# Performance work log

Hardware: AMD Instinct MI355X
Metric: run time of the kernel (lower is better)

## Reference

```python
import jax, jax.numpy as jnp
import numpy as np

B_SI = 4.1491   # neutron scattering length Si (fm)
B_O = 5.803     # neutron scattering length O (fm)
CUTOFF = 3.5    # tetrahedral neighbour cutoff (A)
BIG = 1e6       # masked-distance sentinel (finite to keep grads NaN-free)


def setup_inputs() -> dict:
    key = jax.random.key(0)
    k1, k2 = jax.random.split(key)
    N, L = 4096, 40.0
    positions = jax.random.uniform(k1, (N, 3), dtype=jnp.float32) * L
    cell = (L * jnp.eye(3)).astype(jnp.float32)
    r_bins = (0.05 + 0.05 * jnp.arange(200, dtype=jnp.float32))      # 0.05..10.0 A
    q_bins = jnp.linspace(0.5, 25.0, 500, dtype=jnp.float32)          # A^-1
    species = jax.random.randint(k2, (N,), 0, 3, dtype=jnp.int32)     # 0=Si, 1/2=O
    return {"positions": positions, "cell": cell, "r_bins": r_bins,
            "q_bins": q_bins, "species": species}


def _pair_geometry(positions, cell):
    # Minimum-image displacements under a general periodic cell.
    disp = positions[:, None, :] - positions[None, :, :]        # [N,N,3]
    frac = disp @ jnp.linalg.inv(cell)
    frac = frac - jnp.round(frac)
    disp = frac @ cell
    d2 = jnp.sum(disp * disp, axis=-1)                           # [N,N]
    self_mask = jnp.eye(positions.shape[0], dtype=bool)
    dist = jnp.sqrt(jnp.where(self_mask, 1.0, d2))               # safe sqrt on diag
    return disp, dist, self_mask


def reference(positions, cell, r_bins, q_bins, species):
    N = positions.shape[0]
    nbins = r_bins.shape[0]
    dtype = positions.dtype

    disp, dist, self_mask = _pair_geometry(positions, cell)

    # --- neutron-weighted G(r): differentiable linear (cloud-in-cell) binning ---
    b = jnp.where(species == 0, B_SI, B_O).astype(dtype)         # per-atom scattering length
    w = (b[:, None] * b[None, :]) / (jnp.mean(b) ** 2)           # Faber-Ziman pair weights
    r0, dr = r_bins[0], r_bins[1] - r_bins[0]
    x = (dist - r0) / dr
    i0 = jnp.floor(x).astype(jnp.int32)
    f = x - i0.astype(dtype)
    valid = (~self_mask) & (i0 >= 0) & (i0 < nbins - 1)
    w0 = jnp.where(valid, w * (1.0 - f), 0.0).ravel()
    w1 = jnp.where(valid, w * f, 0.0).ravel()
    i0f = jnp.clip(i0, 0, nbins - 1).ravel()
    hist = (jnp.zeros(nbins, dtype)
            .at[i0f].add(w0)
            .at[jnp.clip(i0f + 1, 0, nbins - 1)].add(w1))
    V = jnp.abs(jnp.linalg.det(cell))
    rho = N / V
    shell = 4.0 * jnp.pi * r_bins ** 2 * dr                       # ideal-gas shell volume
    G_r = hist / (N * rho * shell)                                # [nbins]

    # --- total correlation function T(r) = 4 pi rho r G(r) ---
    T_r = 4.0 * jnp.pi * rho * r_bins * G_r

    # --- structure factor S(Q) = 1 + 4 pi rho int r^2 (G(r)-1) sinc(Qr) dr ---
    qr = q_bins[:, None] * r_bins[None, :]                        # [nQ, nr]
    integrand = (r_bins ** 2) * (G_r - 1.0)
    S_Q = 1.0 + 4.0 * jnp.pi * rho * dr * jnp.sum(
        integrand[None, :] * jnp.sinc(qr / jnp.pi), axis=1)

    # --- tetrahedral order parameter q_tet over Si centres with O neighbours ---
    central = species == 0
    nbr_ok = (species != 0)[None, :] & (~self_mask)
    nd = jnp.where(nbr_ok, dist, BIG)
    negd, idx = jax.lax.top_k(-nd, 4)                             # 4 nearest O per atom
    d4 = -negd                                                    # [N,4]
    u = jnp.take_along_axis(disp, idx[:, :, None], axis=1) / d4[:, :, None]  # unit vecs
    cosang = jnp.einsum('nkd,nld->nkl', u, u)                     # [N,4,4]
    pair_mask = jnp.triu(jnp.ones((4, 4), bool), 1)               # 6 angle pairs
    q_i = 1.0 - (3.0 / 8.0) * jnp.sum(((cosang + 1.0 / 3.0) ** 2) * pair_mask, axis=(1, 2))
    vf = (central & (d4[:, 3] < CUTOFF)).astype(dtype)            # needs 4 nbrs in cutoff
    q_tet = jnp.sum(q_i * vf) / jnp.maximum(jnp.sum(vf), 1.0)

    return G_r, T_r, S_Q, q_tet
```

## Files before the change

### kernel.cpp

```cpp
#include <hip/hip_runtime.h>
#include <climits>
#include <math.h>


#define B_SI_F 4.1491f
#define B_O_F  5.803f
#define CUTOFF_F 3.5f
#define CUT_SLACK 3.5005f
#define NCOPIES 16
#define CAP 32

#define WS_HIST 16
#define WS_CNT  4096

__device__ __forceinline__ bool dless(float da, int ia, float db, int ib) {
    return (da < db) || (da == db && ia < ib);
}

struct CellK {
    float ci0, ci1, ci2, ci3, ci4, ci5, ci6, ci7, ci8;
    float c0, c1, c2, c3, c4, c5, c6, c7, c8;
};

__device__ __forceinline__ CellK make_cell(const float* __restrict__ cellm,
                                           bool& diag) {
    CellK K;
    K.c0 = cellm[0]; K.c1 = cellm[1]; K.c2 = cellm[2];
    K.c3 = cellm[3]; K.c4 = cellm[4]; K.c5 = cellm[5];
    K.c6 = cellm[6]; K.c7 = cellm[7]; K.c8 = cellm[8];
    double m0 = K.c0, m1 = K.c1, m2 = K.c2;
    double m3 = K.c3, m4 = K.c4, m5 = K.c5;
    double m6 = K.c6, m7 = K.c7, m8 = K.c8;
    double det = m0*(m4*m8 - m5*m7) - m1*(m3*m8 - m5*m6) + m2*(m3*m7 - m4*m6);
    double rd = 1.0 / det;
    K.ci0 = (float)( (m4*m8 - m5*m7) * rd);
    K.ci1 = (float)(-(m1*m8 - m2*m7) * rd);
    K.ci2 = (float)( (m1*m5 - m2*m4) * rd);
    K.ci3 = (float)(-(m3*m8 - m5*m6) * rd);
    K.ci4 = (float)( (m0*m8 - m2*m6) * rd);
    K.ci5 = (float)(-(m0*m5 - m2*m3) * rd);
    K.ci6 = (float)( (m3*m7 - m4*m6) * rd);
    K.ci7 = (float)(-(m0*m7 - m1*m6) * rd);
    K.ci8 = (float)( (m0*m4 - m1*m3) * rd);
    diag = (K.c1 == 0.0f) && (K.c2 == 0.0f) && (K.c3 == 0.0f) &&
           (K.c5 == 0.0f) && (K.c6 == 0.0f) && (K.c7 == 0.0f);
    return K;
}

template<bool DIAG>
__device__ __forceinline__ void min_image(const CellK& K,
                                          float dx, float dy, float dz,
                                          float& ex, float& ey, float& ez) {
    if (DIAG) {
        float t0 = dx * K.ci0, t1 = dy * K.ci4, t2 = dz * K.ci8;
        t0 -= rintf(t0);  t1 -= rintf(t1);  t2 -= rintf(t2);
        ex = t0 * K.c0;  ey = t1 * K.c4;  ez = t2 * K.c8;
    } else {
        float f0 = dx*K.ci0 + dy*K.ci3 + dz*K.ci6;
        float f1 = dx*K.ci1 + dy*K.ci4 + dz*K.ci7;
        float f2 = dx*K.ci2 + dy*K.ci5 + dz*K.ci8;
        f0 -= rintf(f0);  f1 -= rintf(f1);  f2 -= rintf(f2);
        ex = f0*K.c0 + f1*K.c3 + f2*K.c6;
        ey = f0*K.c1 + f1*K.c4 + f2*K.c7;
        ez = f0*K.c2 + f1*K.c5 + f2*K.c8;
    }
}

template<bool DIAG>
__device__ __forceinline__ void hist_sweep(const CellK& K,
                                           const float4* __restrict__ sj,
                                           int lbase, int jb0,
                                           float xi, float yi, float zi, float wi,
                                           float rb0, float inv_dr, int nbins_m1,
                                           float* shist,
                                           bool iSi, bool iO, bool offdiag, int iidx,
                                           float* __restrict__ cnt,
                                           int* __restrict__ cand) {
    #pragma unroll 4
    for (int l = 0; l < 32; ++l) {
        const float4 pj = sj[lbase + l];
        float ex, ey, ez;
        min_image<DIAG>(K, xi - pj.x, yi - pj.y, zi - pj.z, ex, ey, ez);
        float dist = __builtin_amdgcn_sqrtf(fmaf(ex, ex, fmaf(ey, ey, ez * ez)));
        float x  = (dist - rb0) * inv_dr;
        float fl = floorf(x);
        int   i0 = (int)fl;
        if (i0 >= 0 && i0 < nbins_m1) {
            float w = wi * pj.w;
            float f = x - fl;
            atomicAdd(&shist[i0],     w * (1.0f - f));
            atomicAdd(&shist[i0 + 1], w * f);
        }
        if (dist < CUT_SLACK) {
            const int jg = jb0 + lbase + l;
            if (iSi && pj.w == B_O_F) {
                float old = atomicAdd(&cnt[iidx], 1.0f);
                int slot = (int)rintf(old);
                if (slot < CAP) cand[iidx * CAP + slot] = jg;
            }
            if (offdiag && iO && pj.w == B_SI_F) {
                float old = atomicAdd(&cnt[jg], 1.0f);
                int slot = (int)rintf(old);
                if (slot < CAP) cand[jg * CAP + slot] = iidx;
            }
        }
    }
}

__global__ __launch_bounds__(256) void k_main(const float* __restrict__ cellm,
                                              const float* __restrict__ pos,
                                              const int* __restrict__ species,
                                              const float* __restrict__ rbins,
                                              float* __restrict__ ws,
                                              int N, int nbins, int T) {
    const int tid = threadIdx.x;
    const int bid = blockIdx.x;

    bool diag;
    const CellK K = make_cell(cellm, diag);

    __shared__ float shist[256];
    __shared__ float sjf[64 * 4];
    shist[tid] = 0.0f;

    const int jhalf = bid & 1;
    int rem = bid >> 1;
    int ti = 0;
    while (rem >= T - ti) { rem -= T - ti; ti++; }
    const int tj = ti + rem;
    const int jb0 = tj * 128 + jhalf * 64;

    if (tid < 192) {
        int g = 3 * jb0 + tid;
        float v = (g < 3 * N) ? pos[g] : 0.0f;
        sjf[(tid / 3) * 4 + (tid % 3)] = v;
    } else {
        int a = tid - 192;
        int ja = jb0 + a;
        float b = (ja < N) ? ((species[ja] == 0) ? B_SI_F : B_O_F) : 0.0f;
        sjf[a * 4 + 3] = b;
    }

    const float rb0     = rbins[0];
    const float inv_dr  = 1.0f / (rbins[1] - rbins[0]);
    const int   nbins_m1 = nbins - 1;

    const int il  = tid & 127;
    const int sub = tid >> 7;
    const int i   = ti * 128 + il;
    const int ig  = min(i, N - 1);
    const float xi = pos[3*ig], yi = pos[3*ig+1], zi = pos[3*ig+2];
    const int   spi = species[ig];
    const float b_i = (spi == 0) ? B_SI_F : B_O_F;
    const float wmul = (ti == tj) ? 1.0f : 2.0f;
    const float wi = (i < N) ? b_i * wmul : 0.0f;
    const bool iSi = (i < N) && (spi == 0);
    const bool iO  = (i < N) && (spi != 0);
    const bool offdiag = (ti != tj);

    float* cnt  = ws + WS_CNT;
    int*   cand = (int*)(ws + WS_CNT + 3 * (size_t)N);

    __syncthreads();

    const float4* sj = (const float4*)sjf;
    if (diag) hist_sweep<true >(K, sj, sub * 32, jb0, xi, yi, zi, wi, rb0, inv_dr, nbins_m1, shist, iSi, iO, offdiag, i, cnt, cand);
    else      hist_sweep<false>(K, sj, sub * 32, jb0, xi, yi, zi, wi, rb0, inv_dr, nbins_m1, shist, iSi, iO, offdiag, i, cnt, cand);

    __syncthreads();

    float* gh = ws + WS_HIST + (size_t)(bid % NCOPIES) * nbins;
    for (int t = tid; t < nbins; t += 256) {
        float h = shist[t];
        if (h != 0.0f) atomicAdd(&gh[t], h);
    }
}

template<bool DIAG>
__device__ __forceinline__ void top4_sweep_s(const CellK& K,
                                             const float* __restrict__ pos,
                                             const int* __restrict__ species,
                                             int N, int lane, int self,
                                             float xi, float yi, float zi,
                                             float& e0, float& e1, float& e2, float& e3,
                                             int& j0, int& j1, int& j2, int& j3) {
    for (int k = lane; k < N; k += 64) {
        int   sp = species[k];
        float px = pos[3*k], py = pos[3*k+1], pz = pos[3*k+2];
        float ex, ey, ez;
        min_image<DIAG>(K, xi - px, yi - py, zi - pz, ex, ey, ez);
        float d2 = fmaf(ex, ex, fmaf(ey, ey, ez * ez));
        float c  = (sp != 0 && k != self) ? d2 : 1e30f;
        int   jc = k;
        if (dless(c, jc, e3, j3)) {
            bool lt2 = dless(c, jc, e2, j2);
            bool lt1 = dless(c, jc, e1, j1);
            bool lt0 = dless(c, jc, e0, j0);
            e3 = lt2 ? e2 : c;               j3 = lt2 ? j2 : jc;
            e2 = lt2 ? (lt1 ? e1 : c) : e2;  j2 = lt2 ? (lt1 ? j1 : jc) : j2;
            e1 = lt1 ? (lt0 ? e0 : c) : e1;  j1 = lt1 ? (lt0 ? j0 : jc) : j1;
            e0 = lt0 ? c : e0;               j0 = lt0 ? jc : j0;
        }
    }
}

__global__ __launch_bounds__(256) void k_tet(const float* __restrict__ cellm,
                                             const float* __restrict__ pos,
                                             const int* __restrict__ species,
                                             float* __restrict__ ws, int N) {
    const int s = __builtin_amdgcn_readfirstlane(blockIdx.x * 4 + (threadIdx.x >> 6));
    if (s >= N) return;
    const int lane = threadIdx.x & 63;

    float* cnt = ws + WS_CNT;
    float* qv  = ws + WS_CNT + N;
    const int* cand = (const int*)(ws + WS_CNT + 3 * (size_t)N);

    if (species[s] != 0) {
        if (lane == 0) { qv[2*s] = 0.0f; qv[2*s + 1] = 0.0f; }
        return;
    }

    bool diag;
    const CellK K = make_cell(cellm, diag);
    const float xi = pos[3*s], yi = pos[3*s+1], zi = pos[3*s+2];

    const int c = (int)rintf(cnt[s]);
    if (lane == 0) cnt[s] = 0.0f;

    float e0 = 1e30f, e1 = 1e30f, e2 = 1e30f, e3 = 1e30f;
    int   j0 = INT_MAX, j1 = INT_MAX, j2 = INT_MAX, j3 = INT_MAX;

    if (c <= CAP) {
        if (lane < c) {
            int j = cand[s * CAP + lane];
            float ex, ey, ez;
            if (diag) min_image<true >(K, xi - pos[3*j], yi - pos[3*j+1], zi - pos[3*j+2], ex, ey, ez);
            else      min_image<false>(K, xi - pos[3*j], yi - pos[3*j+1], zi - pos[3*j+2], ex, ey, ez);
            e0 = fmaf(ex, ex, fmaf(ey, ey, ez * ez));
            j0 = j;
        }
    } else {
        if (diag) top4_sweep_s<true >(K, pos, species, N, lane, s, xi, yi, zi, e0, e1, e2, e3, j0, j1, j2, j3);
        else      top4_sweep_s<false>(K, pos, species, N, lane, s, xi, yi, zi, e0, e1, e2, e3, j0, j1, j2, j3);
    }

    float r0d, r1d, r2d, r3d;  int r0j, r1j, r2j, r3j;
    #define EXTRACT_MIN(RD, RJ)                                        \
    {                                                                  \
        float md = e0; int mj = j0;                                    \
        for (int off = 32; off > 0; off >>= 1) {                       \
            float od = __shfl_xor(md, off, 64);                        \
            int   oj = __shfl_xor(mj, off, 64);                        \
            bool keep = dless(md, mj, od, oj);                         \
            md = keep ? md : od;                                       \
            mj = keep ? mj : oj;                                       \
        }                                                              \
        RD = md; RJ = mj;                                              \
        bool pop = (j0 == mj);                                         \
        e0 = pop ? e1 : e0;  j0 = pop ? j1 : j0;                       \
        e1 = pop ? e2 : e1;  j1 = pop ? j2 : j1;                       \
        e2 = pop ? e3 : e2;  j2 = pop ? j3 : j2;                       \
        e3 = pop ? 1e30f : e3;  j3 = pop ? INT_MAX : j3;               \
    }
    EXTRACT_MIN(r0d, r0j)
    EXTRACT_MIN(r1d, r1j)
    EXTRACT_MIN(r2d, r2j)
    EXTRACT_MIN(r3d, r3j)
    #undef EXTRACT_MIN

    if (lane == 0) {
        float qiv = 0.0f, vf = 0.0f;
        if (r3j != INT_MAX) {
            float dd0 = sqrtf(r0d), dd1 = sqrtf(r1d), dd2 = sqrtf(r2d), dd3 = sqrtf(r3d);
            if (dd3 < CUTOFF_F) {
                float ux[4], uy[4], uz[4];
                float dd[4]  = {dd0, dd1, dd2, dd3};
                int   jj4[4] = {r0j, r1j, r2j, r3j};
                #pragma unroll
                for (int k = 0; k < 4; ++k) {
                    int jk = jj4[k];
                    float ex, ey, ez;
                    if (diag) min_image<true >(K, xi - pos[3*jk], yi - pos[3*jk+1], zi - pos[3*jk+2], ex, ey, ez);
                    else      min_image<false>(K, xi - pos[3*jk], yi - pos[3*jk+1], zi - pos[3*jk+2], ex, ey, ez);
                    ux[k] = ex / dd[k];
                    uy[k] = ey / dd[k];
                    uz[k] = ez / dd[k];
                }
                float s2 = 0.0f;
                #pragma unroll
                for (int k = 0; k < 4; ++k)
                    #pragma unroll
                    for (int l = k + 1; l < 4; ++l) {
                        float cs = ux[k]*ux[l] + uy[k]*uy[l] + uz[k]*uz[l];
                        float t  = cs + (1.0f / 3.0f);
                        s2 += t * t;
                    }
                qiv = 1.0f - 0.375f * s2;
                vf  = 1.0f;
            }
        }
        qv[2*s]     = qiv;
        qv[2*s + 1] = vf;
    }
}

__device__ __forceinline__ float fast_sinc(float x) {
    float rev = x * 0.15915494309189535f;
    rev -= rintf(rev);
    float sn = __builtin_amdgcn_sinf(rev);
    return sn * __builtin_amdgcn_rcpf(x);
}

__global__ __launch_bounds__(256) void k_finalize(const float* __restrict__ cellm,
                                                  const float* __restrict__ ws,
                                                  const float* __restrict__ rbins,
                                                  const float* __restrict__ qbins,
                                                  const int* __restrict__ species,
                                                  float* __restrict__ out,
                                                  int N, int nbins, int nq) {
    __shared__ float2 srw[256];
    __shared__ float rq[256], rv[256];
    __shared__ int   scnt[256];
    const int tid = threadIdx.x;

    double m0 = cellm[0], m1 = cellm[1], m2 = cellm[2];
    double m3 = cellm[3], m4 = cellm[4], m5 = cellm[5];
    double m6 = cellm[6], m7 = cellm[7], m8 = cellm[8];
    double det = m0*(m4*m8 - m5*m7) - m1*(m3*m8 - m5*m6) + m2*(m3*m7 - m4*m6);
    const float rho = (float)((double)N / fabs(det));

    {
        int c = 0;
        for (int k = tid; k < N; k += 256) c += (species[k] == 0) ? 1 : 0;
        scnt[tid] = c;
    }
    __syncthreads();
    for (int s = 128; s > 0; s >>= 1) {
        if (tid < s) scnt[tid] += scnt[tid + s];
        __syncthreads();
    }
    const int nSi = scnt[0];
    const float mean_b  = ((float)nSi * B_SI_F + (float)(N - nSi) * B_O_F) / (float)N;
    const float w_scale = 1.0f / (mean_b * mean_b);

    const float dr  = rbins[1] - rbins[0];
    const float FOURPI = 4.0f * 3.14159265358979323846f;

    for (int t = tid; t < nbins; t += blockDim.x) {
        float h = 0.0f;
        #pragma unroll
        for (int c = 0; c < NCOPIES; ++c) h += ws[WS_HIST + c * nbins + t];
        h *= w_scale;
        float r = rbins[t];
        float shell = FOURPI * r * r * dr;
        float g = h / ((float)N * rho * shell);
        srw[t] = make_float2(r, r * r * (g - 1.0f));
        if (blockIdx.x == 0) {
            out[t] = g;
            out[nbins + t] = FOURPI * rho * r * g;
        }
    }

    if (blockIdx.x == 0) {
        const float* qv = ws + WS_CNT + N;
        float sq = 0.0f, sv = 0.0f;
        for (int s = tid; s < N; s += 256) {
            sq += qv[2*s];
            sv += qv[2*s + 1];
        }
        rq[tid] = sq; rv[tid] = sv;
    }
    __syncthreads();
    if (blockIdx.x == 0) {
        for (int s = 128; s > 0; s >>= 1) {
            if (tid < s) { rq[tid] += rq[tid + s]; rv[tid] += rv[tid + s]; }
            __syncthreads();
        }
        if (tid == 0)
            out[2 * nbins + nq] = rq[0] / fmaxf(rv[0], 1.0f);
    }

    int q = blockIdx.x * blockDim.x + tid;
    if (q < nq) {
        float qq = qbins[q];
        float s0 = 0.0f, s1 = 0.0f, s2 = 0.0f, s3 = 0.0f;
        int t = 0;
        for (; t + 4 <= nbins; t += 4) {
            float2 a = srw[t], b = srw[t+1], c = srw[t+2], d = srw[t+3];
            s0 += a.y * fast_sinc(qq * a.x);
            s1 += b.y * fast_sinc(qq * b.x);
            s2 += c.y * fast_sinc(qq * c.x);
            s3 += d.y * fast_sinc(qq * d.x);
        }
        for (; t < nbins; ++t) {
            float2 a = srw[t];
            s0 += a.y * fast_sinc(qq * a.x);
        }
        float s = (s0 + s1) + (s2 + s3);
        out[2 * nbins + q] = 1.0f + FOURPI * rho * dr * s;
    }
}

extern "C" void kernel_launch(void* const* d_in, const int* in_sizes, int n_in,
                              void* d_out, int out_size, void* d_ws, size_t ws_size,
                              hipStream_t stream) {
    const float* pos     = (const float*)d_in[0];
    const float* cell    = (const float*)d_in[1];
    const float* rbins   = (const float*)d_in[2];
    const float* qbins   = (const float*)d_in[3];
    const int*   species = (const int*)d_in[4];
    float* out = (float*)d_out;
    float* ws  = (float*)d_ws;

    const int N     = in_sizes[4];
    const int nbins = in_sizes[2];
    const int nq    = in_sizes[3];

    const int T  = (N + 127) / 128;
    const int P2 = T * (T + 1);
    const int BT = (N + 3) / 4;
    const int QB = (nq + 255) / 256;

    k_main<<<P2, 256, 0, stream>>>(cell, pos, species, rbins, ws, N, nbins, T);
    k_tet<<<BT, 256, 0, stream>>>(cell, pos, species, ws, N);
    k_finalize<<<QB, 256, 0, stream>>>(cell, ws, rbins, qbins, species, out, N, nbins, nq);
}
```

Measured before the change: 96.84 us.

## Fuse tet kernel into finalize, precompute fractional coords, replicate shared histograms

The main pair kernel now handles a full 128x128 tile per block with half the blocks. It precomputes fractional coordinates for both atom sets so each pair needs only a subtract and rint. Shared-memory histogram atomics are spread across four replicas to reduce contention, and the neighbour cutoff test uses squared distance. The separate q_tet kernel is merged into the finalize launch as extra blocks that reduce through global atomics with a last-block counter, removing one launch and the per-atom q buffer. The extra workspace counters must reset correctly across calls, and the larger tiles mean fewer blocks to fill the device.

```diff
diff --git a/kernel.cpp b/kernel.cpp
--- a/kernel.cpp
+++ b/kernel.cpp
@@ -6,7 +6,7 @@
 #define B_SI_F 4.1491f
 #define B_O_F  5.803f
 #define CUTOFF_F 3.5f
-#define CUT_SLACK 3.5005f
+#define CS2 12.25350025f
 #define NCOPIES 16
 #define CAP 32
 
@@ -70,28 +70,38 @@
 __device__ __forceinline__ void hist_sweep(const CellK& K,
                                            const float4* __restrict__ sj,
                                            int lbase, int jb0,
-                                           float xi, float yi, float zi, float wi,
-                                           float rb0, float inv_dr, int nbins_m1,
-                                           float* shist,
+                                           float fi0, float fi1, float fi2,
+                                           float wi, float inv_dr, float nrb0,
+                                           int nbins_m1, float* shc,
                                            bool iSi, bool iO, bool offdiag, int iidx,
                                            float* __restrict__ cnt,
                                            int* __restrict__ cand) {
     #pragma unroll 4
-    for (int l = 0; l < 32; ++l) {
+    for (int l = 0; l < 64; ++l) {
         const float4 pj = sj[lbase + l];
+        float d0 = fi0 - pj.x;  d0 -= rintf(d0);
+        float d1 = fi1 - pj.y;  d1 -= rintf(d1);
+        float d2 = fi2 - pj.z;  d2 -= rintf(d2);
         float ex, ey, ez;
-        min_image<DIAG>(K, xi - pj.x, yi - pj.y, zi - pj.z, ex, ey, ez);
-        float dist = __builtin_amdgcn_sqrtf(fmaf(ex, ex, fmaf(ey, ey, ez * ez)));
-        float x  = (dist - rb0) * inv_dr;
+        if (DIAG) {
+            ex = d0 * K.c0;  ey = d1 * K.c4;  ez = d2 * K.c8;
+        } else {
+            ex = d0*K.c0 + d1*K.c3 + d2*K.c6;
+            ey = d0*K.c1 + d1*K.c4 + d2*K.c7;
+            ez = d0*K.c2 + d1*K.c5 + d2*K.c8;
+        }
+        float dsq  = fmaf(ex, ex, fmaf(ey, ey, ez * ez));
+        float dist = __builtin_amdgcn_sqrtf(dsq);
+        float x  = fmaf(dist, inv_dr, nrb0);
         float fl = floorf(x);
         int   i0 = (int)fl;
-        if (i0 >= 0 && i0 < nbins_m1) {
-            float w = wi * pj.w;
-            float f = x - fl;
-            atomicAdd(&shist[i0],     w * (1.0f - f));
-            atomicAdd(&shist[i0 + 1], w * f);
-        }
-        if (dist < CUT_SLACK) {
+        if ((unsigned)i0 < (unsigned)nbins_m1) {
+            float w  = wi * pj.w;
+            float wf = w * (x - fl);
+            atomicAdd(&shc[i0],     w - wf);
+            atomicAdd(&shc[i0 + 1], wf);
+        }
+        if (dsq < CS2) {
             const int jg = jb0 + lbase + l;
             if (iSi && pj.w == B_O_F) {
                 float old = atomicAdd(&cnt[iidx], 1.0f);
@@ -119,30 +129,40 @@
     bool diag;
     const CellK K = make_cell(cellm, diag);
 
-    __shared__ float shist[256];
-    __shared__ float sjf[64 * 4];
-    shist[tid] = 0.0f;
-
-    const int jhalf = bid & 1;
-    int rem = bid >> 1;
-    int ti = 0;
+    __shared__ float sh[4 * 257];
+    __shared__ float sjf[128 * 4];
+
+    for (int u = tid; u < 4 * 257; u += 256) sh[u] = 0.0f;
+
+    int rem = bid, ti = 0;
     while (rem >= T - ti) { rem -= T - ti; ti++; }
-    const int tj = ti + rem;
-    const int jb0 = tj * 128 + jhalf * 64;
-
-    if (tid < 192) {
-        int g = 3 * jb0 + tid;
-        float v = (g < 3 * N) ? pos[g] : 0.0f;
-        sjf[(tid / 3) * 4 + (tid % 3)] = v;
-    } else {
-        int a = tid - 192;
-        int ja = jb0 + a;
-        float b = (ja < N) ? ((species[ja] == 0) ? B_SI_F : B_O_F) : 0.0f;
-        sjf[a * 4 + 3] = b;
-    }
-
-    const float rb0     = rbins[0];
-    const float inv_dr  = 1.0f / (rbins[1] - rbins[0]);
+    const int tj  = ti + rem;
+    const int jb0 = tj * 128;
+
+    for (int u = tid; u < 384; u += 256) {
+        int g = 3 * jb0 + u;
+        sjf[(u / 3) * 4 + (u % 3)] = (g < 3 * N) ? pos[g] : 0.0f;
+    }
+    if (tid < 128) {
+        int ja = jb0 + tid;
+        sjf[tid * 4 + 3] = (ja < N) ? ((species[ja] == 0) ? B_SI_F : B_O_F) : 0.0f;
+    }
+    __syncthreads();
+    if (tid < 128) {
+        float x = sjf[tid*4], y = sjf[tid*4+1], z = sjf[tid*4+2];
+        float f0, f1, f2;
+        if (diag) { f0 = x*K.ci0; f1 = y*K.ci4; f2 = z*K.ci8; }
+        else {
+            f0 = x*K.ci0 + y*K.ci3 + z*K.ci6;
+            f1 = x*K.ci1 + y*K.ci4 + z*K.ci7;
+            f2 = x*K.ci2 + y*K.ci5 + z*K.ci8;
+        }
+        sjf[tid*4] = f0;  sjf[tid*4+1] = f1;  sjf[tid*4+2] = f2;
+    }
+
+    const float rb0      = rbins[0];
+    const float inv_dr   = 1.0f / (rbins[1] - rbins[0]);
+    const float nrb0     = -rb0 * inv_dr;
     const int   nbins_m1 = nbins - 1;
 
     const int il  = tid & 127;
@@ -150,28 +170,37 @@
     const int i   = ti * 128 + il;
     const int ig  = min(i, N - 1);
     const float xi = pos[3*ig], yi = pos[3*ig+1], zi = pos[3*ig+2];
-    const int   spi = species[ig];
-    const float b_i = (spi == 0) ? B_SI_F : B_O_F;
+    float fi0, fi1, fi2;
+    if (diag) { fi0 = xi*K.ci0; fi1 = yi*K.ci4; fi2 = zi*K.ci8; }
+    else {
+        fi0 = xi*K.ci0 + yi*K.ci3 + zi*K.ci6;
+        fi1 = xi*K.ci1 + yi*K.ci4 + zi*K.ci7;
+        fi2 = xi*K.ci2 + yi*K.ci5 + zi*K.ci8;
+    }
+    const int   spi  = species[ig];
+    const float b_i  = (spi == 0) ? B_SI_F : B_O_F;
     const float wmul = (ti == tj) ? 1.0f : 2.0f;
-    const float wi = (i < N) ? b_i * wmul : 0.0f;
+    const float wi   = (i < N) ? b_i * wmul : 0.0f;
     const bool iSi = (i < N) && (spi == 0);
     const bool iO  = (i < N) && (spi != 0);
     const bool offdiag = (ti != tj);
 
     float* cnt  = ws + WS_CNT;
-    int*   cand = (int*)(ws + WS_CNT + 3 * (size_t)N);
+    int*   cand = (int*)(ws + WS_CNT + N);
+    float* shc  = sh + ((tid >> 4) & 3) * 257;
 
     __syncthreads();
 
     const float4* sj = (const float4*)sjf;
-    if (diag) hist_sweep<true >(K, sj, sub * 32, jb0, xi, yi, zi, wi, rb0, inv_dr, nbins_m1, shist, iSi, iO, offdiag, i, cnt, cand);
-    else      hist_sweep<false>(K, sj, sub * 32, jb0, xi, yi, zi, wi, rb0, inv_dr, nbins_m1, shist, iSi, iO, offdiag, i, cnt, cand);
+    const int lbase = sub * 64;
+    if (diag) hist_sweep<true >(K, sj, lbase, jb0, fi0, fi1, fi2, wi, inv_dr, nrb0, nbins_m1, shc, iSi, iO, offdiag, i, cnt, cand);
+    else      hist_sweep<false>(K, sj, lbase, jb0, fi0, fi1, fi2, wi, inv_dr, nrb0, nbins_m1, shc, iSi, iO, offdiag, i, cnt, cand);
 
     __syncthreads();
 
     float* gh = ws + WS_HIST + (size_t)(bid % NCOPIES) * nbins;
     for (int t = tid; t < nbins; t += 256) {
-        float h = shist[t];
+        float h = sh[t] + sh[257 + t] + sh[514 + t] + sh[771 + t];
         if (h != 0.0f) atomicAdd(&gh[t], h);
     }
 }
@@ -204,107 +233,6 @@
     }
 }
 
-__global__ __launch_bounds__(256) void k_tet(const float* __restrict__ cellm,
-                                             const float* __restrict__ pos,
-                                             const int* __restrict__ species,
-                                             float* __restrict__ ws, int N) {
-    const int s = __builtin_amdgcn_readfirstlane(blockIdx.x * 4 + (threadIdx.x >> 6));
-    if (s >= N) return;
-    const int lane = threadIdx.x & 63;
-
-    float* cnt = ws + WS_CNT;
-    float* qv  = ws + WS_CNT + N;
-    const int* cand = (const int*)(ws + WS_CNT + 3 * (size_t)N);
-
-    if (species[s] != 0) {
-        if (lane == 0) { qv[2*s] = 0.0f; qv[2*s + 1] = 0.0f; }
-        return;
-    }
-
-    bool diag;
-    const CellK K = make_cell(cellm, diag);
-    const float xi = pos[3*s], yi = pos[3*s+1], zi = pos[3*s+2];
-
-    const int c = (int)rintf(cnt[s]);
-    if (lane == 0) cnt[s] = 0.0f;
-
-    float e0 = 1e30f, e1 = 1e30f, e2 = 1e30f, e3 = 1e30f;
-    int   j0 = INT_MAX, j1 = INT_MAX, j2 = INT_MAX, j3 = INT_MAX;
-
-    if (c <= CAP) {
-        if (lane < c) {
-            int j = cand[s * CAP + lane];
-            float ex, ey, ez;
-            if (diag) min_image<true >(K, xi - pos[3*j], yi - pos[3*j+1], zi - pos[3*j+2], ex, ey, ez);
-            else      min_image<false>(K, xi - pos[3*j], yi - pos[3*j+1], zi - pos[3*j+2], ex, ey, ez);
-            e0 = fmaf(ex, ex, fmaf(ey, ey, ez * ez));
-            j0 = j;
-        }
-    } else {
-        if (diag) top4_sweep_s<true >(K, pos, species, N, lane, s, xi, yi, zi, e0, e1, e2, e3, j0, j1, j2, j3);
-        else      top4_sweep_s<false>(K, pos, species, N, lane, s, xi, yi, zi, e0, e1, e2, e3, j0, j1, j2, j3);
-    }
-
-    float r0d, r1d, r2d, r3d;  int r0j, r1j, r2j, r3j;
-    #define EXTRACT_MIN(RD, RJ)                                        \
-    {                                                                  \
-        float md = e0; int mj = j0;                                    \
-        for (int off = 32; off > 0; off >>= 1) {                       \
-            float od = __shfl_xor(md, off, 64);                        \
-            int   oj = __shfl_xor(mj, off, 64);                        \
-            bool keep = dless(md, mj, od, oj);                         \
-            md = keep ? md : od;                                       \
-            mj = keep ? mj : oj;                                       \
-        }                                                              \
-        RD = md; RJ = mj;                                              \
-        bool pop = (j0 == mj);                                         \
-        e0 = pop ? e1 : e0;  j0 = pop ? j1 : j0;                       \
-        e1 = pop ? e2 : e1;  j1 = pop ? j2 : j1;                       \
-        e2 = pop ? e3 : e2;  j2 = pop ? j3 : j2;                       \
-        e3 = pop ? 1e30f : e3;  j3 = pop ? INT_MAX : j3;               \
-    }
-    EXTRACT_MIN(r0d, r0j)
-    EXTRACT_MIN(r1d, r1j)
-    EXTRACT_MIN(r2d, r2j)
-    EXTRACT_MIN(r3d, r3j)
-    #undef EXTRACT_MIN
-
-    if (lane == 0) {
-        float qiv = 0.0f, vf = 0.0f;
-        if (r3j != INT_MAX) {
-            float dd0 = sqrtf(r0d), dd1 = sqrtf(r1d), dd2 = sqrtf(r2d), dd3 = sqrtf(r3d);
-            if (dd3 < CUTOFF_F) {
-                float ux[4], uy[4], uz[4];
-                float dd[4]  = {dd0, dd1, dd2, dd3};
-                int   jj4[4] = {r0j, r1j, r2j, r3j};
-                #pragma unroll
-                for (int k = 0; k < 4; ++k) {
-                    int jk = jj4[k];
-                    float ex, ey, ez;
-                    if (diag) min_image<true >(K, xi - pos[3*jk], yi - pos[3*jk+1], zi - pos[3*jk+2], ex, ey, ez);
-                    else      min_image<false>(K, xi - pos[3*jk], yi - pos[3*jk+1], zi - pos[3*jk+2], ex, ey, ez);
-                    ux[k] = ex / dd[k];
-                    uy[k] = ey / dd[k];
-                    uz[k] = ez / dd[k];
-                }
-                float s2 = 0.0f;
-                #pragma unroll
-                for (int k = 0; k < 4; ++k)
-                    #pragma unroll
-                    for (int l = k + 1; l < 4; ++l) {
-                        float cs = ux[k]*ux[l] + uy[k]*uy[l] + uz[k]*uz[l];
-                        float t  = cs + (1.0f / 3.0f);
-                        s2 += t * t;
-                    }
-                qiv = 1.0f - 0.375f * s2;
-                vf  = 1.0f;
-            }
-        }
-        qv[2*s]     = qiv;
-        qv[2*s + 1] = vf;
-    }
-}
-
 __device__ __forceinline__ float fast_sinc(float x) {
     float rev = x * 0.15915494309189535f;
     rev -= rintf(rev);
@@ -312,17 +240,129 @@
     return sn * __builtin_amdgcn_rcpf(x);
 }
 
-__global__ __launch_bounds__(256) void k_finalize(const float* __restrict__ cellm,
-                                                  const float* __restrict__ ws,
-                                                  const float* __restrict__ rbins,
-                                                  const float* __restrict__ qbins,
-                                                  const int* __restrict__ species,
-                                                  float* __restrict__ out,
-                                                  int N, int nbins, int nq) {
+__global__ __launch_bounds__(256) void k_fin(const float* __restrict__ cellm,
+                                             float* __restrict__ ws,
+                                             const float* __restrict__ rbins,
+                                             const float* __restrict__ qbins,
+                                             const int* __restrict__ species,
+                                             const float* __restrict__ pos,
+                                             float* __restrict__ out,
+                                             int N, int nbins, int nq,
+                                             int QB, int BT) {
+    const int tid = threadIdx.x;
+    const int bid = blockIdx.x;
+
+    if (bid >= QB) {
+        __shared__ float swq[4], swv[4];
+        const int wid  = tid >> 6;
+        const int lane = tid & 63;
+        const int s = __builtin_amdgcn_readfirstlane((bid - QB) * 4 + wid);
+        float* cnt = ws + WS_CNT;
+        const int* cand = (const int*)(ws + WS_CNT + N);
+
+        float qiv = 0.0f, vf = 0.0f;
+        if (s < N && species[s] == 0) {
+            bool diag;
+            const CellK K = make_cell(cellm, diag);
+            const float xi = pos[3*s], yi = pos[3*s+1], zi = pos[3*s+2];
+            const int c = (int)rintf(cnt[s]);
+            if (lane == 0) cnt[s] = 0.0f;
+
+            float e0 = 1e30f, e1 = 1e30f, e2 = 1e30f, e3 = 1e30f;
+            int   j0 = INT_MAX, j1 = INT_MAX, j2 = INT_MAX, j3 = INT_MAX;
+
+            if (c <= CAP) {
+                if (lane < c) {
+                    int j = cand[s * CAP + lane];
+                    float ex, ey, ez;
+                    if (diag) min_image<true >(K, xi - pos[3*j], yi - pos[3*j+1], zi - pos[3*j+2], ex, ey, ez);
+                    else      min_image<false>(K, xi - pos[3*j], yi - pos[3*j+1], zi - pos[3*j+2], ex, ey, ez);
+                    e0 = fmaf(ex, ex, fmaf(ey, ey, ez * ez));
+                    j0 = j;
+                }
+            } else {
+                if (diag) top4_sweep_s<true >(K, pos, species, N, lane, s, xi, yi, zi, e0, e1, e2, e3, j0, j1, j2, j3);
+                else      top4_sweep_s<false>(K, pos, species, N, lane, s, xi, yi, zi, e0, e1, e2, e3, j0, j1, j2, j3);
+            }
+
+            float r0d, r1d, r2d, r3d;  int r0j, r1j, r2j, r3j;
+            #define EXTRACT_MIN(RD, RJ)                                        \
+            {                                                                  \
+                float md = e0; int mj = j0;                                    \
+                for (int off = 32; off > 0; off >>= 1) {                       \
+                    float od = __shfl_xor(md, off, 64);                        \
+                    int   oj = __shfl_xor(mj, off, 64);                        \
+                    bool keep = dless(md, mj, od, oj);                         \
+                    md = keep ? md : od;                                       \
+                    mj = keep ? mj : oj;                                       \
+                }                                                              \
+                RD = md; RJ = mj;                                              \
+                bool pop = (j0 == mj);                                         \
+                e0 = pop ? e1 : e0;  j0 = pop ? j1 : j0;                       \
+                e1 = pop ? e2 : e1;  j1 = pop ? j2 : j1;                       \
+                e2 = pop ? e3 : e2;  j2 = pop ? j3 : j2;                       \
+                e3 = pop ? 1e30f : e3;  j3 = pop ? INT_MAX : j3;               \
+            }
+            EXTRACT_MIN(r0d, r0j)
+            EXTRACT_MIN(r1d, r1j)
+            EXTRACT_MIN(r2d, r2j)
+            EXTRACT_MIN(r3d, r3j)
+            #undef EXTRACT_MIN
+
+            if (lane == 0 && r3j != INT_MAX) {
+                float dd0 = sqrtf(r0d), dd1 = sqrtf(r1d), dd2 = sqrtf(r2d), dd3 = sqrtf(r3d);
+                if (dd3 < CUTOFF_F) {
+                    float ux[4], uy[4], uz[4];
+                    float dd[4]  = {dd0, dd1, dd2, dd3};
+                    int   jj4[4] = {r0j, r1j, r2j, r3j};
+                    #pragma unroll
+                    for (int k = 0; k < 4; ++k) {
+                        int jk = jj4[k];
+                        float ex, ey, ez;
+                        if (diag) min_image<true >(K, xi - pos[3*jk], yi - pos[3*jk+1], zi - pos[3*jk+2], ex, ey, ez);
+                        else      min_image<false>(K, xi - pos[3*jk], yi - pos[3*jk+1], zi - pos[3*jk+2], ex, ey, ez);
+                        ux[k] = ex / dd[k];
+                        uy[k] = ey / dd[k];
+                        uz[k] = ez / dd[k];
+                    }
+                    float s2 = 0.0f;
+                    #pragma unroll
+                    for (int k = 0; k < 4; ++k)
+                        #pragma unroll
+                        for (int l = k + 1; l < 4; ++l) {
+                            float cs = ux[k]*ux[l] + uy[k]*uy[l] + uz[k]*uz[l];
+                            float t  = cs + (1.0f / 3.0f);
+                            s2 += t * t;
+                        }
+                    qiv = 1.0f - 0.375f * s2;
+                    vf  = 1.0f;
+                }
+            }
+        }
+        if (lane == 0) { swq[wid] = qiv; swv[wid] = vf; }
+        __syncthreads();
+        if (tid == 0) {
+            float bsq = swq[0] + swq[1] + swq[2] + swq[3];
+            float bsv = swv[0] + swv[1] + swv[2] + swv[3];
+            atomicAdd(&ws[8], bsq);
+            atomicAdd(&ws[9], bsv);
+            __threadfence();
+            float old = atomicAdd(&ws[10], 1.0f);
+            if (old > (float)BT - 1.5f) {
+                __threadfence();
+                float tq = atomicAdd(&ws[8], 0.0f);
+                float tv = atomicAdd(&ws[9], 0.0f);
+                out[2 * nbins + nq] = tq / fmaxf(tv, 1.0f);
+                atomicExch(&ws[8], 0.0f);
+                atomicExch(&ws[9], 0.0f);
+                atomicExch(&ws[10], 0.0f);
+            }
+        }
+        return;
+    }
+
     __shared__ float2 srw[256];
-    __shared__ float rq[256], rv[256];
-    __shared__ int   scnt[256];
-    const int tid = threadIdx.x;
+    __shared__ int    scnt[256];
 
     double m0 = cellm[0], m1 = cellm[1], m2 = cellm[2];
     double m3 = cellm[3], m4 = cellm[4], m5 = cellm[5];
@@ -344,7 +384,7 @@
     const float mean_b  = ((float)nSi * B_SI_F + (float)(N - nSi) * B_O_F) / (float)N;
     const float w_scale = 1.0f / (mean_b * mean_b);
 
-    const float dr  = rbins[1] - rbins[0];
+    const float dr = rbins[1] - rbins[0];
     const float FOURPI = 4.0f * 3.14159265358979323846f;
 
     for (int t = tid; t < nbins; t += blockDim.x) {
@@ -356,32 +396,14 @@
         float shell = FOURPI * r * r * dr;
         float g = h / ((float)N * rho * shell);
         srw[t] = make_float2(r, r * r * (g - 1.0f));
-        if (blockIdx.x == 0) {
+        if (bid == 0) {
             out[t] = g;
             out[nbins + t] = FOURPI * rho * r * g;
         }
     }
-
-    if (blockIdx.x == 0) {
-        const float* qv = ws + WS_CNT + N;
-        float sq = 0.0f, sv = 0.0f;
-        for (int s = tid; s < N; s += 256) {
-            sq += qv[2*s];
-            sv += qv[2*s + 1];
-        }
-        rq[tid] = sq; rv[tid] = sv;
-    }
     __syncthreads();
-    if (blockIdx.x == 0) {
-        for (int s = 128; s > 0; s >>= 1) {
-            if (tid < s) { rq[tid] += rq[tid + s]; rv[tid] += rv[tid + s]; }
-            __syncthreads();
-        }
-        if (tid == 0)
-            out[2 * nbins + nq] = rq[0] / fmaxf(rv[0], 1.0f);
-    }
-
-    int q = blockIdx.x * blockDim.x + tid;
+
+    int q = bid * blockDim.x + tid;
     if (q < nq) {
         float qq = qbins[q];
         float s0 = 0.0f, s1 = 0.0f, s2 = 0.0f, s3 = 0.0f;
@@ -418,11 +440,10 @@
     const int nq    = in_sizes[3];
 
     const int T  = (N + 127) / 128;
-    const int P2 = T * (T + 1);
+    const int P  = T * (T + 1) / 2;
     const int BT = (N + 3) / 4;
     const int QB = (nq + 255) / 256;
 
-    k_main<<<P2, 256, 0, stream>>>(cell, pos, species, rbins, ws, N, nbins, T);
-    k_tet<<<BT, 256, 0, stream>>>(cell, pos, species, ws, N);
-    k_finalize<<<QB, 256, 0, stream>>>(cell, ws, rbins, qbins, species, out, N, nbins, nq);
-}
+    k_main<<<P, 256, 0, stream>>>(cell, pos, species, rbins, ws, N, nbins, T);
+    k_fin<<<QB + BT, 256, 0, stream>>>(cell, ws, rbins, qbins, species, pos, out, N, nbins, nq, QB, BT);
+}
```

Measured after the change: 123.9 us. +28.0%, slower.
